# Kernel optimization log

Hardware: AMD Instinct MI355X
Metric: run time of the kernel (lower is better)

Reference implementation:

```python
import jax, jax.numpy as jnp
import numpy as np

NUM_EXPERTS = 8
TOP_K = 2
HIDDEN = 2048
INTER = 5632
NUM_TOKENS = 8192


def setup_inputs() -> dict:
    key = jax.random.key(0)
    ks = jax.random.split(key, 5)
    s_h = 1.0 / np.sqrt(HIDDEN)
    s_i = 1.0 / np.sqrt(INTER)
    return {
        "hidden_states": jax.random.normal(ks[0], (NUM_TOKENS, HIDDEN), jnp.float32),
        # router: ReplicatedLinear(hidden, num_experts, bias=False) -> weight [E, H]
        "w_router": jax.random.normal(ks[1], (NUM_EXPERTS, HIDDEN), jnp.float32) * s_h,
        # FusedMoE SiLU-gated MLP per expert: gate/up [E, H, I], down [E, I, H]
        "w_gate": jax.random.normal(ks[2], (NUM_EXPERTS, HIDDEN, INTER), jnp.float32) * s_h,
        "w_up": jax.random.normal(ks[3], (NUM_EXPERTS, HIDDEN, INTER), jnp.float32) * s_h,
        "w_down": jax.random.normal(ks[4], (NUM_EXPERTS, INTER, HIDDEN), jnp.float32) * s_i,
    }


def reference(hidden_states, w_router, w_gate, w_up, w_down):
    x = hidden_states  # [T, H]
    # Router linear (no bias)
    router_logits = x @ w_router.T  # [T, E]
    # FusedMoE topk: softmax over all experts, take top-k, renormalize=False
    probs = jax.nn.softmax(router_logits.astype(jnp.float32), axis=-1)
    topk_w, topk_idx = jax.lax.top_k(probs, TOP_K)  # [T, k]
    topk_w = topk_w.astype(x.dtype)

    out = jnp.zeros_like(x)
    for e in range(NUM_EXPERTS):
        # combine weight for tokens that routed to expert e (0 otherwise)
        w_e = jnp.sum(jnp.where(topk_idx == e, topk_w, 0.0), axis=-1)  # [T]
        h = jax.nn.silu(x @ w_gate[e]) * (x @ w_up[e])  # [T, I]
        out = out + (h @ w_down[e]) * w_e[:, None]
    return out
```

## Files before the change

### kernel.cpp

```cpp
#include <hip/hip_runtime.h>
#include <hip/hip_bf16.h>
#include <cstdint>

#define NTOK 8192
#define NEXP 8
#define HID  2048
#define INTR 5632
#define NT1  44
#define NT2  16

#define TCNT_OFF    4096u
#define SLOT_OFF    65536u
#define T2S_OFF     262144u
#define W2_OFF      393216u
#define LISTS_OFF   524288u
#define WL_OFF      786432u
#define WG_OFF      2097152u
#define WBYTES      184549376u
#define WU_OFF      (WG_OFF + WBYTES)
#define HF_OFF      (WU_OFF + WBYTES)
#define HFBYTES     207618048u
#define XG_OFF      (HF_OFF + HFBYTES)

typedef float f32x4  __attribute__((ext_vector_type(4)));
typedef short s16x8  __attribute__((ext_vector_type(8)));
typedef short s16x4  __attribute__((ext_vector_type(4)));

__device__ __forceinline__ short bfc(float f) {
  __hip_bfloat16 h = __float2bfloat16(f);
  return __builtin_bit_cast(short, h);
}
__device__ __forceinline__ float b2f(short s) {
  unsigned u = ((unsigned)(unsigned short)s) << 16;
  return __builtin_bit_cast(float, u);
}
__device__ __forceinline__ s16x8 pk8(float4 a, float4 b) {
  s16x8 v;
  v[0]=bfc(a.x); v[1]=bfc(a.y); v[2]=bfc(a.z); v[3]=bfc(a.w);
  v[4]=bfc(b.x); v[5]=bfc(b.y); v[6]=bfc(b.z); v[7]=bfc(b.w);
  return v;
}
__device__ __forceinline__ void gload16(const void* g, void* l) {
  __builtin_amdgcn_global_load_lds((const __attribute__((address_space(1))) void*)g,
                                   (__attribute__((address_space(3))) void*)l, 16, 0, 0);
}

#define DSR128(dst, addr, IMM) \
  asm volatile("ds_read_b128 %0, %1 offset:" IMM : "=v"(dst) : "v"(addr))
#define WAITLGKM(N) do { \
  asm volatile("s_waitcnt lgkmcnt(" #N ")" ::: "memory"); \
  __builtin_amdgcn_sched_barrier(0); } while (0)
#define WAITVM(N) do { \
  asm volatile("s_waitcnt vmcnt(" #N ")" ::: "memory"); \
  __builtin_amdgcn_sched_barrier(0); } while (0)

#define MFMA_BF16 __builtin_amdgcn_mfma_f32_16x16x32_bf16

__global__ __launch_bounds__(256, 4) void prep_kernel(
    const float* __restrict__ src, short* __restrict__ dst,
    int KT, int NP, int Nsrc) {
  __shared__ float tile[32 * 132];
  const int b = blockIdx.x;
  const int np = b % NP;
  const int kt = (b / NP) % KT;
  const int e  = b / (NP * KT);
  const int tid = threadIdx.x;
  const float* s = src + (size_t)e * KT * 32 * (size_t)Nsrc + (size_t)kt * 32 * Nsrc + np * 128;
#pragma unroll
  for (int i = 0; i < 4; i++) {
    const int idx = tid + i * 256;
    const int row = idx >> 5, c4 = idx & 31;
    float4 v = *(const float4*)(s + (size_t)row * Nsrc + c4 * 4);
    *(float4*)(tile + row * 132 + c4 * 4) = v;
  }
  __syncthreads();
  short* dbase = dst + ((size_t)(e * KT + kt) * (NP * 8) + np * 8) * 512;
#pragma unroll
  for (int i = 0; i < 2; i++) {
    const int c = tid + i * 256;
    const int lane = c & 63;
    const int nf = c >> 6;
    const int n = nf * 16 + (lane & 15);
    const int kb = (lane >> 4) * 8;
    s16x8 o;
#pragma unroll
    for (int j = 0; j < 8; j++) o[j] = bfc(tile[(kb + j) * 132 + n]);
    *(s16x8*)(dbase + (size_t)c * 8) = o;
  }
}

__global__ void router_kernel(const float* __restrict__ x, const float* __restrict__ wr,
                              int* __restrict__ cnt, int* __restrict__ lists,
                              float* __restrict__ wlists) {
  const int wave = threadIdx.x >> 6;
  const int lane = threadIdx.x & 63;
  const int t = blockIdx.x * 4 + wave;
  if (t >= NTOK) return;
  float acc[NEXP];
#pragma unroll
  for (int e = 0; e < NEXP; e++) acc[e] = 0.f;
  const float* xrow = x + (size_t)t * HID;
#pragma unroll
  for (int j = 0; j < HID / 256; j++) {
    const int k = j * 256 + lane * 4;
    float4 xv = *(const float4*)(xrow + k);
#pragma unroll
    for (int e = 0; e < NEXP; e++) {
      float4 wv = *(const float4*)(wr + e * HID + k);
      acc[e] += xv.x * wv.x + xv.y * wv.y + xv.z * wv.z + xv.w * wv.w;
    }
  }
#pragma unroll
  for (int e = 0; e < NEXP; e++) {
    float v = acc[e];
    for (int off = 32; off; off >>= 1) v += __shfl_xor(v, off, 64);
    acc[e] = v;
  }
  if (lane == 0) {
    float m = acc[0];
#pragma unroll
    for (int e = 1; e < NEXP; e++) m = fmaxf(m, acc[e]);
    float p[NEXP], s = 0.f;
#pragma unroll
    for (int e = 0; e < NEXP; e++) { p[e] = __expf(acc[e] - m); s += p[e]; }
    const float inv = 1.f / s;
    int e1 = 0; float b1 = p[0];
#pragma unroll
    for (int e = 1; e < NEXP; e++) if (p[e] > b1) { b1 = p[e]; e1 = e; }
    int e2 = -1; float b2 = -1.f;
#pragma unroll
    for (int e = 0; e < NEXP; e++) if (e != e1 && p[e] > b2) { b2 = p[e]; e2 = e; }
    const int pos1 = atomicAdd(&cnt[e1], 1);
    lists[e1 * NTOK + pos1] = t; wlists[e1 * NTOK + pos1] = b1 * inv;
    const int pos2 = atomicAdd(&cnt[e2], 1);
    lists[e2 * NTOK + pos2] = t; wlists[e2 * NTOK + pos2] = b2 * inv;
  }
}

__global__ void offsets_kernel(const int* __restrict__ cnt, int* __restrict__ poffs) {
  if (threadIdx.x == 0 && blockIdx.x == 0) {
    int o = 0;
#pragma unroll
    for (int e = 0; e < NEXP; e++) { poffs[e] = o; o += ((cnt[e] + 255) >> 8) << 8; }
    poffs[NEXP] = o;
  }
}

__global__ void slotmap_kernel(const int* __restrict__ cnt, const int* __restrict__ poffs,
                               const int* __restrict__ lists, const float* __restrict__ wlists,
                               int* __restrict__ slotlist, int* __restrict__ tcnt,
                               int* __restrict__ tok2slot, float* __restrict__ w2) {
  const int e = blockIdx.x;
  const int c = cnt[e], base = poffs[e];
  for (int pos = threadIdx.x; pos < c; pos += blockDim.x) {
    const int tok = lists[e * NTOK + pos];
    const int slot = base + pos;
    slotlist[slot] = tok;
    const int j = atomicAdd(&tcnt[tok], 1);
    tok2slot[tok * 2 + j] = slot;
    w2[tok * 2 + j] = wlists[e * NTOK + pos];
  }
}

__global__ __launch_bounds__(256, 4) void gather_kernel(
    const float* __restrict__ x, const int* __restrict__ slotlist,
    short* __restrict__ xg) {
  const int c = blockIdx.x * 256 + threadIdx.x;
  const int cl = c & 63;
  const int fragid = c >> 6;
  const int f = fragid & 15;
  const int kt = (fragid >> 4) & 63;
  const int gmt = fragid >> 10;
  const int tok = slotlist[gmt * 256 + f * 16 + (cl & 15)];
  const float* s = x + (size_t)tok * HID + kt * 32 + (cl >> 4) * 8;
  float4 a = *(const float4*)s, b = *(const float4*)(s + 4);
  *(s16x8*)(xg + (size_t)c * 8) = pk8(a, b);
}

__global__ __launch_bounds__(256, 2) void gemm1_kernel(
    const short* __restrict__ xg, const short* __restrict__ wgb,
    const short* __restrict__ wub, const int* __restrict__ cnt,
    const int* __restrict__ poffs, short* __restrict__ hfrag) {
  const int P = blockIdx.x;
  const int xcd = P & 7, slot = P >> 3;
  const int mt = slot & 63, jj = slot >> 6;
  const int g = jj * 8 + xcd;
  const int e = g / NT1, nt = g % NT1;
  if (mt * 128 >= cnt[e]) return;
  const int gmt = (poffs[e] >> 8) + (mt >> 1);
  const int fhalf = (mt & 1) * 8;
  const int tid = threadIdx.x;
  const int w = tid >> 6, lane = tid & 63;
  const int wm = w >> 1, wn = w & 1;

  __shared__ __align__(16) short Lds[2 * 12288];
  const uint32_t ldsbase = (uint32_t)(uintptr_t)&Lds[0];

  const short* srcA  = xg  + (((size_t)gmt * 64) * 16 + fhalf + w * 2) * 512 + lane * 8;
  const short* srcBg = wgb + (((size_t)e * 64) * 352 + nt * 8 + w * 2) * 512 + lane * 8;
  const short* srcBu = wub + (((size_t)e * 64) * 352 + nt * 8 + w * 2) * 512 + lane * 8;

  const uint32_t roA = wm * 4096 + lane * 16;
  const uint32_t roB = 8192 + wn * 4096 + lane * 16;
  const uint32_t roU = 16384 + wn * 4096 + lane * 16;

  f32x4 accG[4][4], accU[4][4];
#pragma unroll
  for (int i = 0; i < 4; i++)
#pragma unroll
    for (int j = 0; j < 4; j++) {
      accG[i][j] = f32x4{0.f, 0.f, 0.f, 0.f};
      accU[i][j] = f32x4{0.f, 0.f, 0.f, 0.f};
    }

  uint32_t cur = 0;

#define STG1(BOFF) do {                                                         \
    short* d = (short*)Lds + ((BOFF) >> 1);                                     \
    gload16(srcA,        d + w * 1024);                                         \
    gload16(srcA + 512,  d + w * 1024 + 512);                                   \
    gload16(srcBg,       d + 4096 + w * 1024);                                  \
    gload16(srcBg + 512, d + 4096 + w * 1024 + 512);                            \
    gload16(srcBu,       d + 8192 + w * 1024);                                  \
    gload16(srcBu + 512, d + 8192 + w * 1024 + 512);                            \
    srcA += 8192; srcBg += 180224; srcBu += 180224; } while (0)

#define MMQ(NF)                                                                 \
  { __builtin_amdgcn_s_setprio(1);                                              \
    accG[0][NF] = MFMA_BF16(af[0], bgf[NF], accG[0][NF], 0, 0, 0);              \
    accU[0][NF] = MFMA_BF16(af[0], buf4[NF], accU[0][NF], 0, 0, 0);             \
    accG[1][NF] = MFMA_BF16(af[1], bgf[NF], accG[1][NF], 0, 0, 0);              \
    accU[1][NF] = MFMA_BF16(af[1], buf4[NF], accU[1][NF], 0, 0, 0);             \
    accG[2][NF] = MFMA_BF16(af[2], bgf[NF], accG[2][NF], 0, 0, 0);              \
    accU[2][NF] = MFMA_BF16(af[2], buf4[NF], accU[2][NF], 0, 0, 0);             \
    accG[3][NF] = MFMA_BF16(af[3], bgf[NF], accG[3][NF], 0, 0, 0);              \
    accU[3][NF] = MFMA_BF16(af[3], buf4[NF], accU[3][NF], 0, 0, 0);             \
    __builtin_amdgcn_s_setprio(0); }

#define G1_BODY(DOSTG)                                                          \
  {                                                                             \
    WAITVM(0);                                                                  \
    __builtin_amdgcn_s_barrier();                                               \
    const uint32_t rb = ldsbase + cur;                                          \
    s16x8 af[4], bgf[4], buf4[4];                                               \
    DSR128(bgf[0], rb + roB, "0");                                              \
    DSR128(buf4[0], rb + roU, "0");                                             \
    DSR128(af[0], rb + roA, "0");                                               \
    DSR128(af[1], rb + roA, "1024");                                            \
    DSR128(af[2], rb + roA, "2048");                                            \
    DSR128(af[3], rb + roA, "3072");                                            \
    DSR128(bgf[1], rb + roB, "1024");                                           \
    DSR128(buf4[1], rb + roU, "1024");                                          \
    DSR128(bgf[2], rb + roB, "2048");                                           \
    DSR128(buf4[2], rb + roU, "2048");                                          \
    DSR128(bgf[3], rb + roB, "3072");                                           \
    DSR128(buf4[3], rb + roU, "3072");                                          \
    if (DOSTG) { STG1(cur ^ 24576); }                                           \
    WAITLGKM(6);                                                                \
    MMQ(0)                                                                      \
    WAITLGKM(4);                                                                \
    MMQ(1)                                                                      \
    WAITLGKM(2);                                                                \
    MMQ(2)                                                                      \
    WAITLGKM(0);                                                                \
    MMQ(3)                                                                      \
    cur ^= 24576;                                                               \
  }

  STG1(0);
  for (int t = 0; t < 63; ++t) G1_BODY(1)
  G1_BODY(0)
#undef G1_BODY
#undef MMQ
#undef STG1

  short* tr = (short*)Lds;
  __syncthreads();
#pragma unroll
  for (int mf = 0; mf < 4; mf++)
#pragma unroll
    for (int reg = 0; reg < 4; reg++) {
      const int row = wm * 64 + mf * 16 + (lane >> 4) * 4 + reg;
#pragma unroll
      for (int nf = 0; nf < 4; nf++) {
        const int col = wn * 64 + nf * 16 + (lane & 15);
        const float gv = accG[mf][nf][reg];
        const float uv = accU[mf][nf][reg];
        tr[row * 136 + col] = bfc((gv / (1.f + __expf(-gv))) * uv);
      }
    }
  __syncthreads();
  short* hb = hfrag + (((size_t)gmt * 176 + nt * 4) * 16 + fhalf) * 512;
#pragma unroll
  for (int i = 0; i < 8; i++) {
    const int c = tid + i * 256;
    const int cl = c & 63;
    const int f7 = (c >> 6) & 7;
    const int ktl = c >> 9;
    const int rr = f7 * 16 + (cl & 15);
    s16x8 v = *(const s16x8*)(tr + rr * 136 + ktl * 32 + (cl >> 4) * 8);
    *(s16x8*)(hb + ((size_t)ktl * 16 + f7) * 512 + cl * 8) = v;
  }
}

__global__ __launch_bounds__(512, 4) void gemm2_kernel(
    const short* __restrict__ hfrag, const short* __restrict__ wdb,
    const int* __restrict__ cnt, const int* __restrict__ poffs,
    __hip_bfloat16* __restrict__ pout) {
  const int P = blockIdx.x;
  const int xcd = P & 7, r = P >> 3;
  const int nt = r & 15, emq = r >> 4;
  const int gm = emq * 8 + xcd;
  const int e = gm >> 5, mt = gm & 31;
  if (mt * 256 >= cnt[e]) return;
  const int gmt = (poffs[e] >> 8) + mt;
  const int n0 = nt * 128;
  const int tid = threadIdx.x;
  const int w = tid >> 6, lane = tid & 63;
  const int wm = w >> 1, wn = w & 1;

  __shared__ __align__(16) short Lds[2 * 12288];
  const uint32_t ldsbase = (uint32_t)(uintptr_t)&Lds[0];

  const short* srcA = hfrag + (((size_t)gmt * 176) * 16 + w * 2) * 512 + lane * 8;
  const short* srcB = wdb + (((size_t)e * 176) * 128 + nt * 8) * 512 + tid * 8;

  const uint32_t roA = wm * 4096 + lane * 16;
  const uint32_t roB = 16384 + wn * 4096 + lane * 16;

  f32x4 acc[4][4];
#pragma unroll
  for (int i = 0; i < 4; i++)
#pragma unroll
    for (int j = 0; j < 4; j++) acc[i][j] = f32x4{0.f, 0.f, 0.f, 0.f};

  uint32_t cur = 0;

#define STG2(BOFF) do {                                                         \
    short* d = (short*)Lds + ((BOFF) >> 1);                                     \
    gload16(srcA,       d + w * 1024);                                          \
    gload16(srcA + 512, d + w * 1024 + 512);                                    \
    gload16(srcB,       d + 8192 + w * 512);                                    \
    srcA += 8192; srcB += 65536; } while (0)

#define MMQ2(NF)                                                                \
  { __builtin_amdgcn_s_setprio(1);                                              \
    acc[0][NF] = MFMA_BF16(af[0], bf[NF], acc[0][NF], 0, 0, 0);                 \
    acc[1][NF] = MFMA_BF16(af[1], bf[NF], acc[1][NF], 0, 0, 0);                 \
    acc[2][NF] = MFMA_BF16(af[2], bf[NF], acc[2][NF], 0, 0, 0);                 \
    acc[3][NF] = MFMA_BF16(af[3], bf[NF], acc[3][NF], 0, 0, 0);                 \
    __builtin_amdgcn_s_setprio(0); }

#define G2_BODY(DOSTG)                                                          \
  {                                                                             \
    WAITVM(0);                                                                  \
    __builtin_amdgcn_s_barrier();                                               \
    const uint32_t rb = ldsbase + cur;                                          \
    s16x8 af[4], bf[4];                                                         \
    DSR128(bf[0], rb + roB, "0");                                               \
    DSR128(af[0], rb + roA, "0");                                               \
    DSR128(af[1], rb + roA, "1024");                                            \
    DSR128(af[2], rb + roA, "2048");                                            \
    DSR128(af[3], rb + roA, "3072");                                            \
    DSR128(bf[1], rb + roB, "1024");                                            \
    DSR128(bf[2], rb + roB, "2048");                                            \
    DSR128(bf[3], rb + roB, "3072");                                            \
    if (DOSTG) { STG2(cur ^ 24576); }                                           \
    WAITLGKM(3);                                                                \
    MMQ2(0)                                                                     \
    WAITLGKM(2);                                                                \
    MMQ2(1)                                                                     \
    WAITLGKM(1);                                                                \
    MMQ2(2)                                                                     \
    WAITLGKM(0);                                                                \
    MMQ2(3)                                                                     \
    cur ^= 24576;                                                               \
  }

  STG2(0);
  for (int t = 0; t < 175; ++t) G2_BODY(1)
  G2_BODY(0)
#undef G2_BODY
#undef MMQ2
#undef STG2

  const int slotb = poffs[e] + mt * 256;
#pragma unroll
  for (int mf = 0; mf < 4; mf++) {
#pragma unroll
    for (int reg = 0; reg < 4; reg++) {
      const int row = wm * 64 + mf * 16 + (lane >> 4) * 4 + reg;
      __hip_bfloat16* op = pout + (size_t)(slotb + row) * HID + n0 + wn * 64 + (lane & 15);
#pragma unroll
      for (int nf = 0; nf < 4; nf++)
        op[nf * 16] = __float2bfloat16(acc[mf][nf][reg]);
    }
  }
}

__global__ __launch_bounds__(256, 8) void combine_kernel(
    const __hip_bfloat16* __restrict__ pout, const int* __restrict__ tok2slot,
    const float* __restrict__ w2, float* __restrict__ out) {
  const int t = blockIdx.x;
  const int s0 = tok2slot[2 * t], s1 = tok2slot[2 * t + 1];
  const float w0 = w2[2 * t], w1 = w2[2 * t + 1];
  const short* p0 = (const short*)pout + (size_t)s0 * HID;
  const short* p1 = (const short*)pout + (size_t)s1 * HID;
  float* o = out + (size_t)t * HID;
  const int i = threadIdx.x;
  s16x8 a = *(const s16x8*)(p0 + i * 8);
  s16x8 b = *(const s16x8*)(p1 + i * 8);
  float4 r0, r1;
  r0.x = w0 * b2f(a[0]) + w1 * b2f(b[0]);
  r0.y = w0 * b2f(a[1]) + w1 * b2f(b[1]);
  r0.z = w0 * b2f(a[2]) + w1 * b2f(b[2]);
  r0.w = w0 * b2f(a[3]) + w1 * b2f(b[3]);
  r1.x = w0 * b2f(a[4]) + w1 * b2f(b[4]);
  r1.y = w0 * b2f(a[5]) + w1 * b2f(b[5]);
  r1.z = w0 * b2f(a[6]) + w1 * b2f(b[6]);
  r1.w = w0 * b2f(a[7]) + w1 * b2f(b[7]);
  *(float4*)(o + i * 8) = r0;
  *(float4*)(o + i * 8 + 4) = r1;
}

extern "C" void kernel_launch(void* const* d_in, const int* in_sizes, int n_in,
                              void* d_out, int out_size, void* d_ws, size_t ws_size,
                              hipStream_t stream) {
  const float* x  = (const float*)d_in[0];
  const float* wr = (const float*)d_in[1];
  const float* wg = (const float*)d_in[2];
  const float* wu = (const float*)d_in[3];
  const float* wd = (const float*)d_in[4];
  float* out = (float*)d_out;
  char* ws = (char*)d_ws;

  int* cnt      = (int*)ws;
  int* poffs    = (int*)(ws + 64);
  int* tcnt     = (int*)(ws + TCNT_OFF);
  int* slotlist = (int*)(ws + SLOT_OFF);
  int* tok2slot = (int*)(ws + T2S_OFF);
  float* w2     = (float*)(ws + W2_OFF);
  int* lists    = (int*)(ws + LISTS_OFF);
  float* wlists = (float*)(ws + WL_OFF);
  short* wgb    = (short*)(ws + WG_OFF);
  short* wub    = (short*)(ws + WU_OFF);
  short* wdb    = (short*)(ws + WG_OFF);
  short* hfrag  = (short*)(ws + HF_OFF);
  short* xg     = (short*)(ws + XG_OFF);
  __hip_bfloat16* pout = (__hip_bfloat16*)(ws + XG_OFF);

  hipMemsetAsync(ws, 0, 256, stream);
  hipMemsetAsync(ws + TCNT_OFF, 0, 32768, stream);
  hipMemsetAsync(ws + SLOT_OFF, 0, 73728, stream);

  router_kernel<<<NTOK / 4, 256, 0, stream>>>(x, wr, cnt, lists, wlists);
  offsets_kernel<<<1, 64, 0, stream>>>(cnt, poffs);
  slotmap_kernel<<<NEXP, 256, 0, stream>>>(cnt, poffs, lists, wlists, slotlist, tcnt, tok2slot, w2);
  gather_kernel<<<18432, 256, 0, stream>>>(x, slotlist, xg);
  prep_kernel<<<NEXP * 64 * 44, 256, 0, stream>>>(wg, wgb, 64, 44, INTR);
  prep_kernel<<<NEXP * 64 * 44, 256, 0, stream>>>(wu, wub, 64, 44, INTR);
  gemm1_kernel<<<8 * 64 * NT1, 256, 0, stream>>>(xg, wgb, wub, cnt, poffs, hfrag);
  prep_kernel<<<NEXP * 176 * 16, 256, 0, stream>>>(wd, wdb, 176, 16, HID);
  gemm2_kernel<<<8 * 16 * 32, 512, 0, stream>>>(hfrag, wdb, cnt, poffs, pout);
  combine_kernel<<<NTOK, 256, 0, stream>>>(pout, tok2slot, w2, out);
}
```

Measured before the change: 1.752 ms.

## Enlarge gemm1 to 256-row tiles with 512 threads and triple-buffer both GEMMs

New measurement: 1.670 ms. 4.7% less time.

```diff
diff --git a/kernel.cpp b/kernel.cpp
--- a/kernel.cpp
+++ b/kernel.cpp
@@ -177,32 +177,31 @@
   *(s16x8*)(xg + (size_t)c * 8) = pk8(a, b);
 }
 
-__global__ __launch_bounds__(256, 2) void gemm1_kernel(
+__global__ __launch_bounds__(512, 1) void gemm1_kernel(
     const short* __restrict__ xg, const short* __restrict__ wgb,
     const short* __restrict__ wub, const int* __restrict__ cnt,
     const int* __restrict__ poffs, short* __restrict__ hfrag) {
   const int P = blockIdx.x;
   const int xcd = P & 7, slot = P >> 3;
-  const int mt = slot & 63, jj = slot >> 6;
+  const int mt = slot & 31, jj = slot >> 5;
   const int g = jj * 8 + xcd;
   const int e = g / NT1, nt = g % NT1;
-  if (mt * 128 >= cnt[e]) return;
-  const int gmt = (poffs[e] >> 8) + (mt >> 1);
-  const int fhalf = (mt & 1) * 8;
+  if (mt * 256 >= cnt[e]) return;
+  const int gmt = (poffs[e] >> 8) + mt;
   const int tid = threadIdx.x;
   const int w = tid >> 6, lane = tid & 63;
   const int wm = w >> 1, wn = w & 1;
 
-  __shared__ __align__(16) short Lds[2 * 12288];
+  __shared__ __align__(16) short Lds[3 * 16384];
   const uint32_t ldsbase = (uint32_t)(uintptr_t)&Lds[0];
 
-  const short* srcA  = xg  + (((size_t)gmt * 64) * 16 + fhalf + w * 2) * 512 + lane * 8;
-  const short* srcBg = wgb + (((size_t)e * 64) * 352 + nt * 8 + w * 2) * 512 + lane * 8;
-  const short* srcBu = wub + (((size_t)e * 64) * 352 + nt * 8 + w * 2) * 512 + lane * 8;
+  const short* srcA  = xg  + (size_t)gmt * 64 * 16 * 512 + tid * 8;
+  const short* srcBg = wgb + (((size_t)e * 64) * 352 + nt * 8) * 512 + tid * 8;
+  const short* srcBu = wub + (((size_t)e * 64) * 352 + nt * 8) * 512 + tid * 8;
 
   const uint32_t roA = wm * 4096 + lane * 16;
-  const uint32_t roB = 8192 + wn * 4096 + lane * 16;
-  const uint32_t roU = 16384 + wn * 4096 + lane * 16;
+  const uint32_t roB = 16384 + wn * 4096 + lane * 16;
+  const uint32_t roU = 24576 + wn * 4096 + lane * 16;
 
   f32x4 accG[4][4], accU[4][4];
 #pragma unroll
@@ -213,49 +212,39 @@
       accU[i][j] = f32x4{0.f, 0.f, 0.f, 0.f};
     }
 
-  uint32_t cur = 0;
-
-#define STG1(BOFF) do {                                                         \
-    short* d = (short*)Lds + ((BOFF) >> 1);                                     \
-    gload16(srcA,        d + w * 1024);                                         \
-    gload16(srcA + 512,  d + w * 1024 + 512);                                   \
-    gload16(srcBg,       d + 4096 + w * 1024);                                  \
-    gload16(srcBg + 512, d + 4096 + w * 1024 + 512);                            \
-    gload16(srcBu,       d + 8192 + w * 1024);                                  \
-    gload16(srcBu + 512, d + 8192 + w * 1024 + 512);                            \
+#define STG1(WB) do {                                                           \
+    short* d = (short*)Lds + ((WB) >> 1);                                       \
+    gload16(srcA,          d + w * 512);                                        \
+    gload16(srcA + 4096,   d + 4096 + w * 512);                                 \
+    gload16(srcBg,         d + 8192 + w * 512);                                 \
+    gload16(srcBu,         d + 12288 + w * 512);                                \
     srcA += 8192; srcBg += 180224; srcBu += 180224; } while (0)
 
 #define MMQ(NF)                                                                 \
   { __builtin_amdgcn_s_setprio(1);                                              \
-    accG[0][NF] = MFMA_BF16(af[0], bgf[NF], accG[0][NF], 0, 0, 0);              \
-    accU[0][NF] = MFMA_BF16(af[0], buf4[NF], accU[0][NF], 0, 0, 0);             \
-    accG[1][NF] = MFMA_BF16(af[1], bgf[NF], accG[1][NF], 0, 0, 0);              \
-    accU[1][NF] = MFMA_BF16(af[1], buf4[NF], accU[1][NF], 0, 0, 0);             \
-    accG[2][NF] = MFMA_BF16(af[2], bgf[NF], accG[2][NF], 0, 0, 0);              \
-    accU[2][NF] = MFMA_BF16(af[2], buf4[NF], accU[2][NF], 0, 0, 0);             \
-    accG[3][NF] = MFMA_BF16(af[3], bgf[NF], accG[3][NF], 0, 0, 0);              \
-    accU[3][NF] = MFMA_BF16(af[3], buf4[NF], accU[3][NF], 0, 0, 0);             \
+    accG[0][NF] = MFMA_BF16(af[0], bg[NF], accG[0][NF], 0, 0, 0);               \
+    accU[0][NF] = MFMA_BF16(af[0], bu[NF], accU[0][NF], 0, 0, 0);               \
+    accG[1][NF] = MFMA_BF16(af[1], bg[NF], accG[1][NF], 0, 0, 0);               \
+    accU[1][NF] = MFMA_BF16(af[1], bu[NF], accU[1][NF], 0, 0, 0);               \
+    accG[2][NF] = MFMA_BF16(af[2], bg[NF], accG[2][NF], 0, 0, 0);               \
+    accU[2][NF] = MFMA_BF16(af[2], bu[NF], accU[2][NF], 0, 0, 0);               \
+    accG[3][NF] = MFMA_BF16(af[3], bg[NF], accG[3][NF], 0, 0, 0);               \
+    accU[3][NF] = MFMA_BF16(af[3], bu[NF], accU[3][NF], 0, 0, 0);               \
     __builtin_amdgcn_s_setprio(0); }
 
-#define G1_BODY(DOSTG)                                                          \
+#define G1_BODY(RB, WB, VMN, DOSTG)                                             \
   {                                                                             \
-    WAITVM(0);                                                                  \
+    WAITVM(VMN);                                                                \
     __builtin_amdgcn_s_barrier();                                               \
-    const uint32_t rb = ldsbase + cur;                                          \
-    s16x8 af[4], bgf[4], buf4[4];                                               \
-    DSR128(bgf[0], rb + roB, "0");                                              \
-    DSR128(buf4[0], rb + roU, "0");                                             \
-    DSR128(af[0], rb + roA, "0");                                               \
-    DSR128(af[1], rb + roA, "1024");                                            \
-    DSR128(af[2], rb + roA, "2048");                                            \
-    DSR128(af[3], rb + roA, "3072");                                            \
-    DSR128(bgf[1], rb + roB, "1024");                                           \
-    DSR128(buf4[1], rb + roU, "1024");                                          \
-    DSR128(bgf[2], rb + roB, "2048");                                           \
-    DSR128(buf4[2], rb + roU, "2048");                                          \
-    DSR128(bgf[3], rb + roB, "3072");                                           \
-    DSR128(buf4[3], rb + roU, "3072");                                          \
-    if (DOSTG) { STG1(cur ^ 24576); }                                           \
+    const uint32_t rb = ldsbase + (RB);                                         \
+    s16x8 af[4], bg[4], bu[4];                                                  \
+    DSR128(bg[0], rb + roB, "0");    DSR128(bu[0], rb + roU, "0");              \
+    DSR128(af[0], rb + roA, "0");    DSR128(af[1], rb + roA, "1024");           \
+    DSR128(af[2], rb + roA, "2048"); DSR128(af[3], rb + roA, "3072");           \
+    DSR128(bg[1], rb + roB, "1024"); DSR128(bu[1], rb + roU, "1024");           \
+    DSR128(bg[2], rb + roB, "2048"); DSR128(bu[2], rb + roU, "2048");           \
+    DSR128(bg[3], rb + roB, "3072"); DSR128(bu[3], rb + roU, "3072");           \
+    if (DOSTG) { STG1(WB); }                                                    \
     WAITLGKM(6);                                                                \
     MMQ(0)                                                                      \
     WAITLGKM(4);                                                                \
@@ -264,12 +253,19 @@
     MMQ(2)                                                                      \
     WAITLGKM(0);                                                                \
     MMQ(3)                                                                      \
-    cur ^= 24576;                                                               \
   }
 
   STG1(0);
-  for (int t = 0; t < 63; ++t) G1_BODY(1)
-  G1_BODY(0)
+  STG1(32768);
+  for (int it = 0; it < 20; ++it) {
+    G1_BODY(0,     65536, 4, 1)
+    G1_BODY(32768, 0,     4, 1)
+    G1_BODY(65536, 32768, 4, 1)
+  }
+  G1_BODY(0,     65536, 4, 1)
+  G1_BODY(32768, 0,     4, 1)
+  G1_BODY(65536, 0,     4, 0)
+  G1_BODY(0,     0,     0, 0)
 #undef G1_BODY
 #undef MMQ
 #undef STG1
@@ -290,16 +286,16 @@
       }
     }
   __syncthreads();
-  short* hb = hfrag + (((size_t)gmt * 176 + nt * 4) * 16 + fhalf) * 512;
+  short* hb = hfrag + (((size_t)gmt * 176 + nt * 4) * 16) * 512;
 #pragma unroll
   for (int i = 0; i < 8; i++) {
-    const int c = tid + i * 256;
+    const int c = tid + i * 512;
     const int cl = c & 63;
-    const int f7 = (c >> 6) & 7;
-    const int ktl = c >> 9;
-    const int rr = f7 * 16 + (cl & 15);
+    const int f = (c >> 6) & 15;
+    const int ktl = c >> 10;
+    const int rr = f * 16 + (cl & 15);
     s16x8 v = *(const s16x8*)(tr + rr * 136 + ktl * 32 + (cl >> 4) * 8);
-    *(s16x8*)(hb + ((size_t)ktl * 16 + f7) * 512 + cl * 8) = v;
+    *(s16x8*)(hb + ((size_t)ktl * 16 + f) * 512 + cl * 8) = v;
   }
 }
 
@@ -319,10 +315,10 @@
   const int w = tid >> 6, lane = tid & 63;
   const int wm = w >> 1, wn = w & 1;
 
-  __shared__ __align__(16) short Lds[2 * 12288];
+  __shared__ __align__(16) short Lds[3 * 12288];
   const uint32_t ldsbase = (uint32_t)(uintptr_t)&Lds[0];
 
-  const short* srcA = hfrag + (((size_t)gmt * 176) * 16 + w * 2) * 512 + lane * 8;
+  const short* srcA = hfrag + (size_t)gmt * 176 * 16 * 512 + tid * 8;
   const short* srcB = wdb + (((size_t)e * 176) * 128 + nt * 8) * 512 + tid * 8;
 
   const uint32_t roA = wm * 4096 + lane * 16;
@@ -334,13 +330,11 @@
 #pragma unroll
     for (int j = 0; j < 4; j++) acc[i][j] = f32x4{0.f, 0.f, 0.f, 0.f};
 
-  uint32_t cur = 0;
-
-#define STG2(BOFF) do {                                                         \
-    short* d = (short*)Lds + ((BOFF) >> 1);                                     \
-    gload16(srcA,       d + w * 1024);                                          \
-    gload16(srcA + 512, d + w * 1024 + 512);                                    \
-    gload16(srcB,       d + 8192 + w * 512);                                    \
+#define STG2(WB) do {                                                           \
+    short* d = (short*)Lds + ((WB) >> 1);                                       \
+    gload16(srcA,        d + w * 512);                                          \
+    gload16(srcA + 4096, d + 4096 + w * 512);                                   \
+    gload16(srcB,        d + 8192 + w * 512);                                   \
     srcA += 8192; srcB += 65536; } while (0)
 
 #define MMQ2(NF)                                                                \
@@ -351,21 +345,19 @@
     acc[3][NF] = MFMA_BF16(af[3], bf[NF], acc[3][NF], 0, 0, 0);                 \
     __builtin_amdgcn_s_setprio(0); }
 
-#define G2_BODY(DOSTG)                                                          \
+#define G2_BODY(RB, WB, VMN, DOSTG)                                             \
   {                                                                             \
-    WAITVM(0);                                                                  \
+    WAITVM(VMN);                                                                \
     __builtin_amdgcn_s_barrier();                                               \
-    const uint32_t rb = ldsbase + cur;                                          \
+    const uint32_t rb = ldsbase + (RB);                                         \
     s16x8 af[4], bf[4];                                                         \
     DSR128(bf[0], rb + roB, "0");                                               \
-    DSR128(af[0], rb + roA, "0");                                               \
-    DSR128(af[1], rb + roA, "1024");                                            \
-    DSR128(af[2], rb + roA, "2048");                                            \
-    DSR128(af[3], rb + roA, "3072");                                            \
+    DSR128(af[0], rb + roA, "0");    DSR128(af[1], rb + roA, "1024");           \
+    DSR128(af[2], rb + roA, "2048"); DSR128(af[3], rb + roA, "3072");           \
     DSR128(bf[1], rb + roB, "1024");                                            \
     DSR128(bf[2], rb + roB, "2048");                                            \
     DSR128(bf[3], rb + roB, "3072");                                            \
-    if (DOSTG) { STG2(cur ^ 24576); }                                           \
+    if (DOSTG) { STG2(WB); }                                                    \
     WAITLGKM(3);                                                                \
     MMQ2(0)                                                                     \
     WAITLGKM(2);                                                                \
@@ -374,12 +366,17 @@
     MMQ2(2)                                                                     \
     WAITLGKM(0);                                                                \
     MMQ2(3)                                                                     \
-    cur ^= 24576;                                                               \
   }
 
   STG2(0);
-  for (int t = 0; t < 175; ++t) G2_BODY(1)
-  G2_BODY(0)
+  STG2(24576);
+  for (int it = 0; it < 58; ++it) {
+    G2_BODY(0,     49152, 3, 1)
+    G2_BODY(24576, 0,     3, 1)
+    G2_BODY(49152, 24576, 3, 1)
+  }
+  G2_BODY(0,     0, 3, 0)
+  G2_BODY(24576, 0, 0, 0)
 #undef G2_BODY
 #undef MMQ2
 #undef STG2
@@ -459,7 +456,7 @@
   gather_kernel<<<18432, 256, 0, stream>>>(x, slotlist, xg);
   prep_kernel<<<NEXP * 64 * 44, 256, 0, stream>>>(wg, wgb, 64, 44, INTR);
   prep_kernel<<<NEXP * 64 * 44, 256, 0, stream>>>(wu, wub, 64, 44, INTR);
-  gemm1_kernel<<<8 * 64 * NT1, 256, 0, stream>>>(xg, wgb, wub, cnt, poffs, hfrag);
+  gemm1_kernel<<<8 * 32 * NT1, 512, 0, stream>>>(xg, wgb, wub, cnt, poffs, hfrag);
   prep_kernel<<<NEXP * 176 * 16, 256, 0, stream>>>(wd, wdb, 176, 16, HID);
   gemm2_kernel<<<8 * 16 * 32, 512, 0, stream>>>(hfrag, wdb, cnt, poffs, pout);
   combine_kernel<<<NTOK, 256, 0, stream>>>(pout, tok2slot, w2, out);
```
